# Performance work log

Hardware: AMD Instinct MI355X
Metric: run time of the kernel (lower is better)

The kernel has to match this reference:

```python
import jax, jax.numpy as jnp
import numpy as np

NU, NI, E = 100000, 100000, 500000  # users, items, edges per edge type
DIN, DH, DOUT = 128, 256, 128


def setup_inputs() -> dict:
    key = jax.random.key(0)
    ks = jax.random.split(key, 18)
    f = lambda k, s: jax.random.normal(k, s, dtype=jnp.float32) * 0.02
    inp = {
        # node embedding tables (x_dict defaults to embedding weights)
        'emb_user': f(ks[0], (NU, DIN)),
        'emb_item': f(ks[1], (NI, DIN)),
        # conv1 params: relation user->item (dst=item) and item->user (dst=user)
        'W1_self_ui': f(ks[2], (DIN, DH)), 'W1_neigh_ui': f(ks[3], (DIN, DH)), 'b1_ui': jnp.zeros((DH,), jnp.float32),
        'W1_self_iu': f(ks[4], (DIN, DH)), 'W1_neigh_iu': f(ks[5], (DIN, DH)), 'b1_iu': jnp.zeros((DH,), jnp.float32),
        # conv2 params
        'W2_self_ui': f(ks[6], (DH, DOUT)), 'W2_neigh_ui': f(ks[7], (DH, DOUT)), 'b2_ui': jnp.zeros((DOUT,), jnp.float32),
        'W2_self_iu': f(ks[8], (DH, DOUT)), 'W2_neigh_iu': f(ks[9], (DH, DOUT)), 'b2_iu': jnp.zeros((DOUT,), jnp.float32),
        # edge lists: e1 = user->item edges, e2 = item->user edges
        'e1_src': jax.random.randint(ks[10], (E,), 0, NU),
        'e1_dst': jax.random.randint(ks[11], (E,), 0, NI),
        'e2_src': jax.random.randint(ks[12], (E,), 0, NI),
        'e2_dst': jax.random.randint(ks[13], (E,), 0, NU),
    }
    return inp


def _sage(h_src, h_dst, e_src, e_dst, W_self, W_neigh, b, n_dst):
    # DGL SAGEConv('mean'): fc_self(h_dst) + fc_neigh(mean_neighbors(h_src)) + bias
    msg = h_src[e_src]                                   # [E, d] gather
    ssum = jax.ops.segment_sum(msg, e_dst, num_segments=n_dst)          # [n_dst, d]
    deg = jax.ops.segment_sum(jnp.ones((e_src.shape[0], 1), h_src.dtype), e_dst, num_segments=n_dst)
    mean = ssum / jnp.maximum(deg, 1.0)                  # zero in-degree -> 0
    return h_dst @ W_self + mean @ W_neigh + b


def reference(emb_user, emb_item,
              W1_self_ui, W1_neigh_ui, b1_ui, W1_self_iu, W1_neigh_iu, b1_iu,
              W2_self_ui, W2_neigh_ui, b2_ui, W2_self_iu, W2_neigh_iu, b2_iu,
              e1_src, e1_dst, e2_src, e2_dst):
    # layer 1 (HeteroGraphConv: each ntype receives from exactly one relation)
    h1_item = jax.nn.leaky_relu(_sage(emb_user, emb_item, e1_src, e1_dst, W1_self_ui, W1_neigh_ui, b1_ui, NI))
    h1_user = jax.nn.leaky_relu(_sage(emb_item, emb_user, e2_src, e2_dst, W1_self_iu, W1_neigh_iu, b1_iu, NU))
    # layer 2
    h2_item = _sage(h1_user, h1_item, e1_src, e1_dst, W2_self_ui, W2_neigh_ui, b2_ui, NI)
    h2_user = _sage(h1_item, h1_user, e2_src, e2_dst, W2_self_iu, W2_neigh_iu, b2_iu, NU)
    return (h2_user, h2_item)
```

## Files before the change

kernel.cpp:

```cpp
#include <hip/hip_runtime.h>
#include <stdint.h>

typedef unsigned short u16;
typedef unsigned int   u32;
typedef __attribute__((ext_vector_type(8))) short bf16x8;
typedef __attribute__((ext_vector_type(4))) float f32x4;
typedef __attribute__((ext_vector_type(2))) float f32x2;
typedef __attribute__((ext_vector_type(8))) unsigned short u16x8;

constexpr int NUc = 100000;
constexpr int NIc = 100000;
constexpr int Ec  = 500000;
constexpr int Mrows = 100000;
constexpr int NB  = (100000 + 255) / 256;

__device__ __forceinline__ u16 f2bf(float f) {
  u32 u = __float_as_uint(f);
  u += 0x7fffu + ((u >> 16) & 1u);
  return (u16)(u >> 16);
}
__device__ __forceinline__ float bf2f(u16 h) { return __uint_as_float(((u32)h) << 16); }

__global__ void hist_kernel(const int* __restrict__ e1_dst, const int* __restrict__ e2_dst,
                            int* __restrict__ ideg1, int* __restrict__ ideg2,
                            int* __restrict__ rank1, int* __restrict__ rank2) {
  int i = blockIdx.x * blockDim.x + threadIdx.x;
  const int stride = gridDim.x * blockDim.x;
  for (; i < 2 * Ec; i += stride) {
    if (i < Ec) rank1[i] = atomicAdd(&ideg1[e1_dst[i]], 1);
    else        rank2[i - Ec] = atomicAdd(&ideg2[e2_dst[i - Ec]], 1);
  }
}

constexpr int PREP_B = 4096;
__global__ void prep_cast(const float* __restrict__ eu, const float* __restrict__ ei,
                          const float* __restrict__ W1s_ui, const float* __restrict__ W1n_ui,
                          const float* __restrict__ W1s_iu, const float* __restrict__ W1n_iu,
                          const float* __restrict__ W2s_ui, const float* __restrict__ W2n_ui,
                          const float* __restrict__ W2s_iu, const float* __restrict__ W2n_iu,
                          u16* __restrict__ ue, u16* __restrict__ ie,
                          u16* __restrict__ Wt1_ui, u16* __restrict__ Wt1_iu,
                          u16* __restrict__ Wt2c_u, u16* __restrict__ Wt2c_i) {
  constexpr int N4 = NUc * 128 / 4;
  constexpr int TOT = 2 * N4 + 262144;
  int i = blockIdx.x * blockDim.x + threadIdx.x;
  const int stride = PREP_B * 256;
  for (int t = i; t < TOT; t += stride) {
    if (t < 2 * N4) {
      const float* src = (t < N4) ? eu : ei;
      u16* dst = (t < N4) ? ue : ie;
      int c = (t < N4) ? t : t - N4;
      f32x4 v = __builtin_nontemporal_load(reinterpret_cast<const f32x4*>(src) + c);
      ushort4 o;
      o.x = f2bf(v.x); o.y = f2bf(v.y); o.z = f2bf(v.z); o.w = f2bf(v.w);
      reinterpret_cast<ushort4*>(dst)[c] = o;
    } else {
      int j = t - 2 * N4;
      if (j < 131072) {
        const float* Ws = (j < 65536) ? W1s_ui : W1s_iu;
        const float* Wn = (j < 65536) ? W1n_ui : W1n_iu;
        u16* dst = (j < 65536) ? Wt1_ui : Wt1_iu;
        int q = j & 65535;
        int n = q >> 8, k = q & 255;
        dst[q] = f2bf(k < 128 ? Ws[k * 256 + n] : Wn[(k - 128) * 256 + n]);
      } else {
        int q = j - 131072;
        int which = q >> 16;
        int s = q & 65535;
        int c = s >> 8, k = s & 255;
        float v;
        if (which == 0) v = (c < 128) ? W2n_ui[k * 128 + c] : W2s_iu[k * 128 + (c - 128)];
        else            v = (c < 128) ? W2n_iu[k * 128 + c] : W2s_ui[k * 128 + (c - 128)];
        u16* dst = which ? Wt2c_i : Wt2c_u;
        dst[s] = f2bf(v);
      }
    }
  }
}

__global__ void block_reduce2(const int* __restrict__ ideg1, const int* __restrict__ ideg2,
                              int* __restrict__ bsum1, int* __restrict__ bsum2, int n) {
  const int* deg = blockIdx.y ? ideg2 : ideg1;
  int* bsum = blockIdx.y ? bsum2 : bsum1;
  __shared__ int s[256];
  int t = threadIdx.x, i = blockIdx.x * 256 + t;
  s[t] = (i < n) ? deg[i] : 0;
  __syncthreads();
  for (int st = 128; st > 0; st >>= 1) { if (t < st) s[t] += s[t + st]; __syncthreads(); }
  if (t == 0) bsum[blockIdx.x] = s[0];
}

__global__ void scan_bsums2(const int* __restrict__ bsum1, const int* __restrict__ bsum2,
                            int* __restrict__ bscan1, int* __restrict__ bscan2, int nb) {
  const int* bsum = blockIdx.x ? bsum2 : bsum1;
  int* bscan = blockIdx.x ? bscan2 : bscan1;
  __shared__ int s[512];
  int t = threadIdx.x;
  int v0 = (t < nb) ? bsum[t] : 0;
  s[t] = v0;
  __syncthreads();
  for (int d = 1; d < 512; d <<= 1) {
    int v = (t >= d) ? s[t - d] : 0;
    __syncthreads();
    s[t] += v;
    __syncthreads();
  }
  if (t < nb) bscan[t] = s[t] - v0;
}

__global__ void scan_blocks2(const int* __restrict__ ideg1, const int* __restrict__ ideg2,
                             const int* __restrict__ bscan1, const int* __restrict__ bscan2,
                             int* __restrict__ off1, int* __restrict__ off2, int n) {
  const int* deg = blockIdx.y ? ideg2 : ideg1;
  const int* bscan = blockIdx.y ? bscan2 : bscan1;
  int* off = blockIdx.y ? off2 : off1;
  __shared__ int s[256];
  int t = threadIdx.x, i = blockIdx.x * 256 + t;
  int d = (i < n) ? deg[i] : 0;
  s[t] = d;
  __syncthreads();
  for (int st = 1; st < 256; st <<= 1) {
    int v = (t >= st) ? s[t - st] : 0;
    __syncthreads();
    s[t] += v;
    __syncthreads();
  }
  if (i < n) off[i] = bscan[blockIdx.x] + s[t] - d;
  if (i == 0) off[n] = Ec;
}

__global__ void fill_csr_kernel(const int* __restrict__ e1_src, const int* __restrict__ e1_dst,
                                const int* __restrict__ e2_src, const int* __restrict__ e2_dst,
                                const int* __restrict__ rank1, const int* __restrict__ rank2,
                                const int* __restrict__ off1, const int* __restrict__ off2,
                                int* __restrict__ csr1, int* __restrict__ csr2) {
  int i = blockIdx.x * blockDim.x + threadIdx.x;
  const int stride = gridDim.x * blockDim.x;
  for (; i < 2 * Ec; i += stride) {
    if (i < Ec) {
      int d = __builtin_nontemporal_load(e1_dst + i);
      int r = __builtin_nontemporal_load(rank1 + i);
      csr1[off1[d] + r] = __builtin_nontemporal_load(e1_src + i);
    } else {
      int e = i - Ec;
      int d = __builtin_nontemporal_load(e2_dst + e);
      int r = __builtin_nontemporal_load(rank2 + e);
      csr2[off2[d] + r] = __builtin_nontemporal_load(e2_src + e);
    }
  }
}

template<int FINAL>
__global__ __launch_bounds__(256) void gather_blk(
    const u16* __restrict__ fA, const int* __restrict__ offA, const int* __restrict__ csrA,
    const u16* __restrict__ sA, void* __restrict__ outA,
    const u16* __restrict__ fB, const int* __restrict__ offB, const int* __restrict__ csrB,
    const u16* __restrict__ sB, void* __restrict__ outB)
{
  constexpr int ROWS = 64;
  constexpr int CAP  = 1536;
  constexpr int NBLK = (100000 + ROWS - 1) / ROWS;
  __shared__ int s_off[ROWS + 1];
  __shared__ int s_csr[CAP];

  const int b = blockIdx.x;
  const u16* f; const int* off; const int* csr; const u16* sf; void* out; int r0;
  if (b < NBLK) { f = fA; off = offA; csr = csrA; sf = sA; out = outA; r0 = b * ROWS; }
  else          { f = fB; off = offB; csr = csrB; sf = sB; out = outB; r0 = (b - NBLK) * ROWS; }

  const int tid = threadIdx.x;
  if (tid <= ROWS) s_off[tid] = off[min(r0 + tid, 100000)];
  __syncthreads();
  const int j0 = s_off[0];
  const int nE = s_off[ROWS] - j0;
  const bool inLds = (nE <= CAP);
  if (inLds) {
    for (int j = tid; j < nE; j += 256) s_csr[j] = csr[j0 + j];
  }
  __syncthreads();

  const int w = tid >> 6, lane = tid & 63;
  const int colb = lane << 1;
  for (int rr = w; rr < ROWS; rr += 4) {
    const int r = r0 + rr;
    if (r >= 100000) break;
    const int a0 = s_off[rr], a1 = s_off[rr + 1];
    float ax = 0.f, ay = 0.f;
    int t = a0;
    if (inLds) {
      const int base = a0 - j0;
      int tl = base;
      const int el = a1 - j0;
      for (; tl + 4 <= el; tl += 4) {
        int s0 = s_csr[tl], s1 = s_csr[tl + 1], s2 = s_csr[tl + 2], s3 = s_csr[tl + 3];
        u32 v0 = *reinterpret_cast<const u32*>(f + (size_t)s0 * 128 + colb);
        u32 v1 = *reinterpret_cast<const u32*>(f + (size_t)s1 * 128 + colb);
        u32 v2 = *reinterpret_cast<const u32*>(f + (size_t)s2 * 128 + colb);
        u32 v3 = *reinterpret_cast<const u32*>(f + (size_t)s3 * 128 + colb);
        ax += __uint_as_float(v0 << 16) + __uint_as_float(v1 << 16)
            + __uint_as_float(v2 << 16) + __uint_as_float(v3 << 16);
        ay += __uint_as_float(v0 & 0xffff0000u) + __uint_as_float(v1 & 0xffff0000u)
            + __uint_as_float(v2 & 0xffff0000u) + __uint_as_float(v3 & 0xffff0000u);
      }
      for (; tl < el; ++tl) {
        int s0 = s_csr[tl];
        u32 v0 = *reinterpret_cast<const u32*>(f + (size_t)s0 * 128 + colb);
        ax += __uint_as_float(v0 << 16);
        ay += __uint_as_float(v0 & 0xffff0000u);
      }
    } else {
      for (; t + 4 <= a1; t += 4) {
        int s0 = csr[t], s1 = csr[t + 1], s2 = csr[t + 2], s3 = csr[t + 3];
        u32 v0 = *reinterpret_cast<const u32*>(f + (size_t)s0 * 128 + colb);
        u32 v1 = *reinterpret_cast<const u32*>(f + (size_t)s1 * 128 + colb);
        u32 v2 = *reinterpret_cast<const u32*>(f + (size_t)s2 * 128 + colb);
        u32 v3 = *reinterpret_cast<const u32*>(f + (size_t)s3 * 128 + colb);
        ax += __uint_as_float(v0 << 16) + __uint_as_float(v1 << 16)
            + __uint_as_float(v2 << 16) + __uint_as_float(v3 << 16);
        ay += __uint_as_float(v0 & 0xffff0000u) + __uint_as_float(v1 & 0xffff0000u)
            + __uint_as_float(v2 & 0xffff0000u) + __uint_as_float(v3 & 0xffff0000u);
      }
      for (; t < a1; ++t) {
        int s0 = csr[t];
        u32 v0 = *reinterpret_cast<const u32*>(f + (size_t)s0 * 128 + colb);
        ax += __uint_as_float(v0 << 16);
        ay += __uint_as_float(v0 & 0xffff0000u);
      }
    }
    float rs = 1.0f / fmaxf((float)(a1 - a0), 1.0f);
    if (FINAL) {
      u32 sv = __builtin_nontemporal_load(
          reinterpret_cast<const u32*>(sf + (size_t)r * 128 + colb));
      f32x2 o;
      o.x = ax * rs + __uint_as_float(sv << 16);
      o.y = ay * rs + __uint_as_float(sv & 0xffff0000u);
      __builtin_nontemporal_store(o, reinterpret_cast<f32x2*>((float*)out + (size_t)r * 128 + colb));
    } else {
      u32 o = (u32)f2bf(ax * rs) | ((u32)f2bf(ay * rs) << 16);
      *reinterpret_cast<u32*>((u16*)out + (size_t)r * 128 + colb) = o;
    }
  }
}

__device__ __forceinline__ void glds16(const void* g, void* l) {
  __builtin_amdgcn_global_load_lds((const __attribute__((address_space(1))) void*)g,
                                   (__attribute__((address_space(3))) void*)l, 16, 0, 0);
}

template<int NTAB, int EPI, int AST>
__global__ __launch_bounds__(256) void mfma_gemm2(
    const u16* __restrict__ A0a, const u16* __restrict__ A1a, const u16* __restrict__ Bta,
    const float* __restrict__ biasa, u16* __restrict__ out0a, u16* __restrict__ out1a,
    const u16* __restrict__ A0b, const u16* __restrict__ A1b, const u16* __restrict__ Btb,
    const float* __restrict__ biasb, u16* __restrict__ out0b, u16* __restrict__ out1b,
    int M)
{
  constexpr int K = 256, BK = 32, BM = 128;
  __shared__ __align__(16) u16 smem[8192];
  u16* As = smem;
  u16* Bs = smem + 4096;

  const bool zb = (blockIdx.z != 0);
  const u16* A0 = zb ? A0b : A0a;
  const u16* A1 = zb ? A1b : A1a;
  const u16* Bt = zb ? Btb : Bta;
  const float* bias = zb ? biasb : biasa;

  const int tid  = threadIdx.x;
  const int lane = tid & 63;
  const int w    = tid >> 6;
  const int wr   = w >> 1, wc = w & 1;
  const int gr0  = blockIdx.x * BM;
  const int gc0  = blockIdx.y * BM;

  f32x4 acc[4][4];
  #pragma unroll
  for (int m = 0; m < 4; ++m)
    #pragma unroll
    for (int n = 0; n < 4; ++n) acc[m][n] = (f32x4){0.f, 0.f, 0.f, 0.f};

  const int srow  = lane >> 2;
  const int sslot = lane & 3;

  for (int kt = 0; kt < K; kt += BK) {
    const u16* At = (NTAB == 2 && kt >= 128) ? A1 : A0;
    const int kbase = (NTAB == 2) ? (kt & 127) : kt;
    #pragma unroll
    for (int c = 0; c < 2; ++c) {
      int rl = w * 32 + c * 16 + srow;
      int swz = (sslot ^ ((rl >> 1) & 3)) << 3;
      int grow = gr0 + rl; grow = grow < M ? grow : M - 1;
      glds16(At + (size_t)grow * AST + kbase + swz, As + (size_t)(w * 32 + c * 16) * BK);
      glds16(Bt + (size_t)(gc0 + rl) * K + kt + swz, Bs + (size_t)(w * 32 + c * 16) * BK);
    }
    __syncthreads();

    bf16x8 af[4], bfr[4];
    #pragma unroll
    for (int m = 0; m < 4; ++m) {
      int row = wr * 64 + m * 16 + (lane & 15);
      int idx = (row << 5) + ((((lane >> 4) ^ ((row >> 1) & 3))) << 3);
      af[m] = *reinterpret_cast<const bf16x8*>(As + idx);
    }
    #pragma unroll
    for (int n = 0; n < 4; ++n) {
      int row = wc * 64 + n * 16 + (lane & 15);
      int idx = (row << 5) + ((((lane >> 4) ^ ((row >> 1) & 3))) << 3);
      bfr[n] = *reinterpret_cast<const bf16x8*>(Bs + idx);
    }
    #pragma unroll
    for (int m = 0; m < 4; ++m)
      #pragma unroll
      for (int n = 0; n < 4; ++n)
        acc[m][n] = __builtin_amdgcn_mfma_f32_16x16x32_bf16(af[m], bfr[n], acc[m][n], 0, 0, 0);
    __syncthreads();
  }

  u16* outp;
  if (EPI == 0) outp = zb ? out0b : out0a;
  else          outp = (blockIdx.y == 0) ? (zb ? out0b : out0a) : (zb ? out1b : out1a);
  const bool useBias = (EPI == 0) || (blockIdx.y == 1);
  const bool ntStore = (EPI == 1) && (blockIdx.y == 1);

  const int cLane = lane & 15;
  const int rGrp  = (lane >> 4) << 2;
  for (int s = 0; s < 2; ++s) {
    if (wr == s) {
      #pragma unroll
      for (int n = 0; n < 4; ++n) {
        int lc = wc * 64 + n * 16 + cLane;
        float b = 0.f;
        if (useBias) b = (EPI == 0) ? bias[gc0 + lc] : bias[lc];
        #pragma unroll
        for (int m = 0; m < 4; ++m) {
          int lr = m * 16 + rGrp;
          #pragma unroll
          for (int r = 0; r < 4; ++r) {
            float v = acc[m][n][r] + b;
            if (EPI == 0) v = (v >= 0.f) ? v : 0.01f * v;
            smem[(lr + r) * 128 + lc] = f2bf(v);
          }
        }
      }
    }
    __syncthreads();
    #pragma unroll
    for (int pass = 0; pass < 4; ++pass) {
      int chunk = pass * 256 + tid;
      int row = chunk >> 4, c8 = chunk & 15;
      int G = gr0 + s * 64 + row;
      if (G < M) {
        u16x8 v = *reinterpret_cast<const u16x8*>(smem + row * 128 + c8 * 8);
        if (EPI == 0)
          *reinterpret_cast<u16x8*>(outp + (size_t)G * 256 + gc0 + c8 * 8) = v;
        else if (ntStore)
          __builtin_nontemporal_store(v, reinterpret_cast<u16x8*>(outp + (size_t)G * 128 + c8 * 8));
        else
          *reinterpret_cast<u16x8*>(outp + (size_t)G * 128 + c8 * 8) = v;
      }
    }
    if (s == 0) __syncthreads();
  }
}

extern "C" void kernel_launch(void* const* d_in, const int* in_sizes, int n_in,
                              void* d_out, int out_size, void* d_ws, size_t ws_size,
                              hipStream_t stream) {
  const float* emb_user    = (const float*)d_in[0];
  const float* emb_item    = (const float*)d_in[1];
  const float* W1_self_ui  = (const float*)d_in[2];
  const float* W1_neigh_ui = (const float*)d_in[3];
  const float* b1_ui       = (const float*)d_in[4];
  const float* W1_self_iu  = (const float*)d_in[5];
  const float* W1_neigh_iu = (const float*)d_in[6];
  const float* b1_iu       = (const float*)d_in[7];
  const float* W2_self_ui  = (const float*)d_in[8];
  const float* W2_neigh_ui = (const float*)d_in[9];
  const float* b2_ui       = (const float*)d_in[10];
  const float* W2_self_iu  = (const float*)d_in[11];
  const float* W2_neigh_iu = (const float*)d_in[12];
  const float* b2_iu       = (const float*)d_in[13];
  const int* e1_src = (const int*)d_in[14];
  const int* e1_dst = (const int*)d_in[15];
  const int* e2_src = (const int*)d_in[16];
  const int* e2_dst = (const int*)d_in[17];

  u16* p16 = (u16*)d_ws;
  u16* ue     = p16; p16 += (size_t)NUc * 128;
  u16* ie     = p16; p16 += (size_t)NIc * 128;
  u16* h1i    = p16; p16 += (size_t)NIc * 256;
  u16* h1u    = p16; p16 += (size_t)NUc * 256;
  u16* aggb_i = p16; p16 += (size_t)NIc * 128;
  u16* aggb_u = p16; p16 += (size_t)NUc * 128;
  u16* proj_i2u = p16; p16 += (size_t)NIc * 128;
  u16* self_i   = p16; p16 += (size_t)NIc * 128;
  u16* Wt1_ui  = p16; p16 += 256 * 256;
  u16* Wt1_iu  = p16; p16 += 256 * 256;
  u16* Wt2c_u  = p16; p16 += 256 * 256;
  u16* Wt2c_i  = p16; p16 += 256 * 256;
  u16* proj_u2i = aggb_i;
  u16* self_u   = aggb_u;
  int* ip    = (int*)p16;
  int* ideg1 = ip;  ip += NIc;
  int* ideg2 = ip;  ip += NUc;
  int* off1  = ip;  ip += NIc + 1;
  int* off2  = ip;  ip += NUc + 1;
  int* rank1 = ip;  ip += Ec;
  int* rank2 = ip;  ip += Ec;
  int* csr1  = ip;  ip += Ec;
  int* csr2  = ip;  ip += Ec;
  int* bsum1 = ip;  ip += 512;
  int* bscan1= ip;  ip += 512;
  int* bsum2 = ip;  ip += 512;
  int* bscan2= ip;  ip += 512;

  float* h2_user = (float*)d_out;
  float* h2_item = h2_user + (size_t)NUc * 128;

  dim3 blk(256);
  const int gatherBlocks = 2 * ((100000 + 63) / 64);
  dim3 gemmGrid(782, 2, 2);

  hipMemsetAsync(ideg1, 0, sizeof(int) * (size_t)(NIc + NUc), stream);
  hist_kernel<<<1024, blk, 0, stream>>>(e1_dst, e2_dst, ideg1, ideg2, rank1, rank2);
  prep_cast<<<PREP_B, blk, 0, stream>>>(
      emb_user, emb_item,
      W1_self_ui, W1_neigh_ui, W1_self_iu, W1_neigh_iu,
      W2_self_ui, W2_neigh_ui, W2_self_iu, W2_neigh_iu,
      ue, ie, Wt1_ui, Wt1_iu, Wt2c_u, Wt2c_i);
  block_reduce2<<<dim3(NB, 2), blk, 0, stream>>>(ideg1, ideg2, bsum1, bsum2, NIc);
  scan_bsums2<<<2, 512, 0, stream>>>(bsum1, bsum2, bscan1, bscan2, NB);
  scan_blocks2<<<dim3(NB, 2), blk, 0, stream>>>(ideg1, ideg2, bscan1, bscan2, off1, off2, NIc);
  fill_csr_kernel<<<1024, blk, 0, stream>>>(e1_src, e1_dst, e2_src, e2_dst,
                                            rank1, rank2, off1, off2, csr1, csr2);

  gather_blk<0><<<gatherBlocks, blk, 0, stream>>>(
      ue, off1, csr1, nullptr, aggb_i,
      ie, off2, csr2, nullptr, aggb_u);
  mfma_gemm2<2, 0, 128><<<gemmGrid, blk, 0, stream>>>(
      ie, aggb_i, Wt1_ui, b1_ui, h1i, nullptr,
      ue, aggb_u, Wt1_iu, b1_iu, h1u, nullptr, Mrows);

  mfma_gemm2<1, 1, 256><<<gemmGrid, blk, 0, stream>>>(
      h1u, nullptr, Wt2c_u, b2_iu, proj_u2i, self_u,
      h1i, nullptr, Wt2c_i, b2_ui, proj_i2u, self_i, Mrows);

  gather_blk<1><<<gatherBlocks, blk, 0, stream>>>(
      proj_u2i, off1, csr1, self_i, h2_item,
      proj_i2u, off2, csr2, self_u, h2_user);
}
```

Before: 347.5 us.

## Fuse layer-1 and layer-2 GEMMs, keeping hidden activations in LDS

Replaces the two separate MFMA GEMM launches with one fused kernel. Each block computes a 64-row tile of the layer-1 hidden activations (bias plus leaky ReLU), keeps it in a swizzled LDS slab, and immediately multiplies it by the concatenated layer-2 weights to produce the projection and self outputs. This removes the write and re-read of the 100k x 256 h1 tensors for both node types and one kernel launch. In exchange it uses a smaller M tile with a full 256-wide N per block, which raises LDS use (about 52 KB per block) and may lower occupancy. The workspace layout is also changed so the outputs no longer alias the aggregation buffers that the fused kernel still reads.

```diff
diff --git a/kernel.cpp b/kernel.cpp
--- a/kernel.cpp
+++ b/kernel.cpp
@@ -19,7 +19,6 @@
   u += 0x7fffu + ((u >> 16) & 1u);
   return (u16)(u >> 16);
 }
-__device__ __forceinline__ float bf2f(u16 h) { return __uint_as_float(((u32)h) << 16); }
 
 __global__ void hist_kernel(const int* __restrict__ e1_dst, const int* __restrict__ e2_dst,
                             int* __restrict__ ideg1, int* __restrict__ ideg2,
@@ -186,10 +185,8 @@
     if (r >= 100000) break;
     const int a0 = s_off[rr], a1 = s_off[rr + 1];
     float ax = 0.f, ay = 0.f;
-    int t = a0;
     if (inLds) {
-      const int base = a0 - j0;
-      int tl = base;
+      int tl = a0 - j0;
       const int el = a1 - j0;
       for (; tl + 4 <= el; tl += 4) {
         int s0 = s_csr[tl], s1 = s_csr[tl + 1], s2 = s_csr[tl + 2], s3 = s_csr[tl + 3];
@@ -209,6 +206,7 @@
         ay += __uint_as_float(v0 & 0xffff0000u);
       }
     } else {
+      int t = a0;
       for (; t + 4 <= a1; t += 4) {
         int s0 = csr[t], s1 = csr[t + 1], s2 = csr[t + 2], s3 = csr[t + 3];
         u32 v0 = *reinterpret_cast<const u32*>(f + (size_t)s0 * 128 + colb);
@@ -247,31 +245,38 @@
                                    (__attribute__((address_space(3))) void*)l, 16, 0, 0);
 }
 
-template<int NTAB, int EPI, int AST>
-__global__ __launch_bounds__(256) void mfma_gemm2(
-    const u16* __restrict__ A0a, const u16* __restrict__ A1a, const u16* __restrict__ Bta,
-    const float* __restrict__ biasa, u16* __restrict__ out0a, u16* __restrict__ out1a,
-    const u16* __restrict__ A0b, const u16* __restrict__ A1b, const u16* __restrict__ Btb,
-    const float* __restrict__ biasb, u16* __restrict__ out0b, u16* __restrict__ out1b,
+__global__ __launch_bounds__(256) void fused_gemm(
+    const u16* __restrict__ Xa, const u16* __restrict__ Sa,
+    const u16* __restrict__ W1a, const float* __restrict__ b1a,
+    const u16* __restrict__ W2a, const float* __restrict__ b2a,
+    u16* __restrict__ proja, u16* __restrict__ selfa,
+    const u16* __restrict__ Xb, const u16* __restrict__ Sb,
+    const u16* __restrict__ W1b, const float* __restrict__ b1b,
+    const u16* __restrict__ W2b, const float* __restrict__ b2b,
+    u16* __restrict__ projb, u16* __restrict__ selfb,
     int M)
 {
-  constexpr int K = 256, BK = 32, BM = 128;
-  __shared__ __align__(16) u16 smem[8192];
-  u16* As = smem;
-  u16* Bs = smem + 4096;
+  constexpr int K = 256, BK = 32, BM = 64;
+  __shared__ __align__(16) u16 As[BM * BK];
+  __shared__ __align__(16) u16 Bs[256 * BK];
+  __shared__ __align__(16) u16 slab[BM * 256];
 
   const bool zb = (blockIdx.z != 0);
-  const u16* A0 = zb ? A0b : A0a;
-  const u16* A1 = zb ? A1b : A1a;
-  const u16* Bt = zb ? Btb : Bta;
-  const float* bias = zb ? biasb : biasa;
+  const u16* X   = zb ? Xb : Xa;
+  const u16* S   = zb ? Sb : Sa;
+  const u16* W1  = zb ? W1b : W1a;
+  const float* b1 = zb ? b1b : b1a;
+  const u16* W2  = zb ? W2b : W2a;
+  const float* b2 = zb ? b2b : b2a;
+  u16* proj  = zb ? projb : proja;
+  u16* selfp = zb ? selfb : selfa;
 
   const int tid  = threadIdx.x;
   const int lane = tid & 63;
   const int w    = tid >> 6;
-  const int wr   = w >> 1, wc = w & 1;
   const int gr0  = blockIdx.x * BM;
-  const int gc0  = blockIdx.y * BM;
+  const int rl   = tid >> 2;
+  const int sslot = tid & 3;
 
   f32x4 acc[4][4];
   #pragma unroll
@@ -279,32 +284,32 @@
     #pragma unroll
     for (int n = 0; n < 4; ++n) acc[m][n] = (f32x4){0.f, 0.f, 0.f, 0.f};
 
-  const int srow  = lane >> 2;
-  const int sslot = lane & 3;
-
   for (int kt = 0; kt < K; kt += BK) {
-    const u16* At = (NTAB == 2 && kt >= 128) ? A1 : A0;
-    const int kbase = (NTAB == 2) ? (kt & 127) : kt;
-    #pragma unroll
-    for (int c = 0; c < 2; ++c) {
-      int rl = w * 32 + c * 16 + srow;
+    const u16* At = (kt >= 128) ? S : X;
+    const int kbase = kt & 127;
+    {
       int swz = (sslot ^ ((rl >> 1) & 3)) << 3;
       int grow = gr0 + rl; grow = grow < M ? grow : M - 1;
-      glds16(At + (size_t)grow * AST + kbase + swz, As + (size_t)(w * 32 + c * 16) * BK);
-      glds16(Bt + (size_t)(gc0 + rl) * K + kt + swz, Bs + (size_t)(w * 32 + c * 16) * BK);
+      glds16(At + (size_t)grow * 128 + kbase + swz, As + (size_t)(w * 16) * BK);
+    }
+    #pragma unroll
+    for (int h = 0; h < 4; ++h) {
+      int rb = h * 64 + rl;
+      int swz = (sslot ^ ((rb >> 1) & 3)) << 3;
+      glds16(W1 + (size_t)rb * K + kt + swz, Bs + (size_t)(h * 64 + w * 16) * BK);
     }
     __syncthreads();
 
     bf16x8 af[4], bfr[4];
     #pragma unroll
     for (int m = 0; m < 4; ++m) {
-      int row = wr * 64 + m * 16 + (lane & 15);
+      int row = m * 16 + (lane & 15);
       int idx = (row << 5) + ((((lane >> 4) ^ ((row >> 1) & 3))) << 3);
       af[m] = *reinterpret_cast<const bf16x8*>(As + idx);
     }
     #pragma unroll
     for (int n = 0; n < 4; ++n) {
-      int row = wc * 64 + n * 16 + (lane & 15);
+      int row = w * 64 + n * 16 + (lane & 15);
       int idx = (row << 5) + ((((lane >> 4) ^ ((row >> 1) & 3))) << 3);
       bfr[n] = *reinterpret_cast<const bf16x8*>(Bs + idx);
     }
@@ -316,50 +321,86 @@
     __syncthreads();
   }
 
-  u16* outp;
-  if (EPI == 0) outp = zb ? out0b : out0a;
-  else          outp = (blockIdx.y == 0) ? (zb ? out0b : out0a) : (zb ? out1b : out1a);
-  const bool useBias = (EPI == 0) || (blockIdx.y == 1);
-  const bool ntStore = (EPI == 1) && (blockIdx.y == 1);
-
-  const int cLane = lane & 15;
-  const int rGrp  = (lane >> 4) << 2;
-  for (int s = 0; s < 2; ++s) {
-    if (wr == s) {
+  #pragma unroll
+  for (int n = 0; n < 4; ++n) {
+    int c = w * 64 + n * 16 + (lane & 15);
+    float b = b1[c];
+    #pragma unroll
+    for (int m = 0; m < 4; ++m) {
       #pragma unroll
-      for (int n = 0; n < 4; ++n) {
-        int lc = wc * 64 + n * 16 + cLane;
-        float b = 0.f;
-        if (useBias) b = (EPI == 0) ? bias[gc0 + lc] : bias[lc];
-        #pragma unroll
-        for (int m = 0; m < 4; ++m) {
-          int lr = m * 16 + rGrp;
-          #pragma unroll
-          for (int r = 0; r < 4; ++r) {
-            float v = acc[m][n][r] + b;
-            if (EPI == 0) v = (v >= 0.f) ? v : 0.01f * v;
-            smem[(lr + r) * 128 + lc] = f2bf(v);
-          }
-        }
-      }
-    }
-    __syncthreads();
-    #pragma unroll
-    for (int pass = 0; pass < 4; ++pass) {
-      int chunk = pass * 256 + tid;
-      int row = chunk >> 4, c8 = chunk & 15;
-      int G = gr0 + s * 64 + row;
-      if (G < M) {
-        u16x8 v = *reinterpret_cast<const u16x8*>(smem + row * 128 + c8 * 8);
-        if (EPI == 0)
-          *reinterpret_cast<u16x8*>(outp + (size_t)G * 256 + gc0 + c8 * 8) = v;
-        else if (ntStore)
-          __builtin_nontemporal_store(v, reinterpret_cast<u16x8*>(outp + (size_t)G * 128 + c8 * 8));
-        else
-          *reinterpret_cast<u16x8*>(outp + (size_t)G * 128 + c8 * 8) = v;
-      }
-    }
-    if (s == 0) __syncthreads();
+      for (int r = 0; r < 4; ++r) {
+        int row = m * 16 + ((lane >> 4) << 2) + r;
+        float v = acc[m][n][r] + b;
+        v = (v >= 0.f) ? v : 0.01f * v;
+        int g = (c >> 3) ^ (row & 7);
+        slab[row * 256 + g * 8 + (c & 7)] = f2bf(v);
+        acc[m][n][r] = 0.f;
+      }
+    }
+  }
+  __syncthreads();
+
+  for (int kt = 0; kt < K; kt += BK) {
+    #pragma unroll
+    for (int h = 0; h < 4; ++h) {
+      int rb = h * 64 + rl;
+      int swz = (sslot ^ ((rb >> 1) & 3)) << 3;
+      glds16(W2 + (size_t)rb * K + kt + swz, Bs + (size_t)(h * 64 + w * 16) * BK);
+    }
+    __syncthreads();
+
+    bf16x8 af[4], bfr[4];
+    #pragma unroll
+    for (int m = 0; m < 4; ++m) {
+      int row = m * 16 + (lane & 15);
+      int g = ((kt >> 3) + (lane >> 4)) ^ (row & 7);
+      af[m] = *reinterpret_cast<const bf16x8*>(slab + row * 256 + g * 8);
+    }
+    #pragma unroll
+    for (int n = 0; n < 4; ++n) {
+      int row = w * 64 + n * 16 + (lane & 15);
+      int idx = (row << 5) + ((((lane >> 4) ^ ((row >> 1) & 3))) << 3);
+      bfr[n] = *reinterpret_cast<const bf16x8*>(Bs + idx);
+    }
+    #pragma unroll
+    for (int m = 0; m < 4; ++m)
+      #pragma unroll
+      for (int n = 0; n < 4; ++n)
+        acc[m][n] = __builtin_amdgcn_mfma_f32_16x16x32_bf16(af[m], bfr[n], acc[m][n], 0, 0, 0);
+    __syncthreads();
+  }
+
+  #pragma unroll
+  for (int n = 0; n < 4; ++n) {
+    int c = w * 64 + n * 16 + (lane & 15);
+    float b = (c >= 128) ? b2[c - 128] : 0.f;
+    #pragma unroll
+    for (int m = 0; m < 4; ++m) {
+      #pragma unroll
+      for (int r = 0; r < 4; ++r) {
+        int row = m * 16 + ((lane >> 4) << 2) + r;
+        int g = (c >> 3) ^ (row & 7);
+        slab[row * 256 + g * 8 + (c & 7)] = f2bf(acc[m][n][r] + b);
+      }
+    }
+  }
+  __syncthreads();
+  #pragma unroll
+  for (int p = 0; p < 8; ++p) {
+    int chunk = p * 256 + tid;
+    int row = chunk >> 5;
+    int gg  = chunk & 31;
+    int G = gr0 + row;
+    if (G < M) {
+      int gsw = gg ^ (row & 7);
+      u16x8 v = *reinterpret_cast<const u16x8*>(slab + row * 256 + gsw * 8);
+      int col = gg * 8;
+      if (col < 128)
+        *reinterpret_cast<u16x8*>(proj + (size_t)G * 128 + col) = v;
+      else
+        __builtin_nontemporal_store(v,
+            reinterpret_cast<u16x8*>(selfp + (size_t)G * 128 + (col - 128)));
+    }
   }
 }
 
@@ -386,20 +427,18 @@
   const int* e2_dst = (const int*)d_in[17];
 
   u16* p16 = (u16*)d_ws;
-  u16* ue     = p16; p16 += (size_t)NUc * 128;
-  u16* ie     = p16; p16 += (size_t)NIc * 128;
-  u16* h1i    = p16; p16 += (size_t)NIc * 256;
-  u16* h1u    = p16; p16 += (size_t)NUc * 256;
-  u16* aggb_i = p16; p16 += (size_t)NIc * 128;
-  u16* aggb_u = p16; p16 += (size_t)NUc * 128;
+  u16* ue       = p16; p16 += (size_t)NUc * 128;
+  u16* ie       = p16; p16 += (size_t)NIc * 128;
+  u16* aggb_i   = p16; p16 += (size_t)NIc * 128;
+  u16* aggb_u   = p16; p16 += (size_t)NUc * 128;
+  u16* proj_u2i = p16; p16 += (size_t)NUc * 128;
+  u16* self_u   = p16; p16 += (size_t)NUc * 128;
   u16* proj_i2u = p16; p16 += (size_t)NIc * 128;
   u16* self_i   = p16; p16 += (size_t)NIc * 128;
-  u16* Wt1_ui  = p16; p16 += 256 * 256;
-  u16* Wt1_iu  = p16; p16 += 256 * 256;
-  u16* Wt2c_u  = p16; p16 += 256 * 256;
-  u16* Wt2c_i  = p16; p16 += 256 * 256;
-  u16* proj_u2i = aggb_i;
-  u16* self_u   = aggb_u;
+  u16* Wt1_ui   = p16; p16 += 256 * 256;
+  u16* Wt1_iu   = p16; p16 += 256 * 256;
+  u16* Wt2c_u   = p16; p16 += 256 * 256;
+  u16* Wt2c_i   = p16; p16 += 256 * 256;
   int* ip    = (int*)p16;
   int* ideg1 = ip;  ip += NIc;
   int* ideg2 = ip;  ip += NUc;
@@ -419,7 +458,7 @@
 
   dim3 blk(256);
   const int gatherBlocks = 2 * ((100000 + 63) / 64);
-  dim3 gemmGrid(782, 2, 2);
+  dim3 fusedGrid((100000 + 63) / 64, 1, 2);
 
   hipMemsetAsync(ideg1, 0, sizeof(int) * (size_t)(NIc + NUc), stream);
   hist_kernel<<<1024, blk, 0, stream>>>(e1_dst, e2_dst, ideg1, ideg2, rank1, rank2);
@@ -437,13 +476,10 @@
   gather_blk<0><<<gatherBlocks, blk, 0, stream>>>(
       ue, off1, csr1, nullptr, aggb_i,
       ie, off2, csr2, nullptr, aggb_u);
-  mfma_gemm2<2, 0, 128><<<gemmGrid, blk, 0, stream>>>(
-      ie, aggb_i, Wt1_ui, b1_ui, h1i, nullptr,
-      ue, aggb_u, Wt1_iu, b1_iu, h1u, nullptr, Mrows);
-
-  mfma_gemm2<1, 1, 256><<<gemmGrid, blk, 0, stream>>>(
-      h1u, nullptr, Wt2c_u, b2_iu, proj_u2i, self_u,
-      h1i, nullptr, Wt2c_i, b2_ui, proj_i2u, self_i, Mrows);
+
+  fused_gemm<<<fusedGrid, blk, 0, stream>>>(
+      ie, aggb_i, Wt1_ui, b1_ui, Wt2c_i, b2_ui, proj_i2u, self_i,
+      ue, aggb_u, Wt1_iu, b1_iu, Wt2c_u, b2_iu, proj_u2i, self_u, Mrows);
 
   gather_blk<1><<<gatherBlocks, blk, 0, stream>>>(
       proj_u2i, off1, csr1, self_i, h2_item,
```

After: 342.1 us. No clear change (-1.6%).
